# Kernel tuning notes

Hardware: AMD Instinct MI355X
Metric: run time of the kernel (lower is better)

Reference implementation:

```python
import jax, jax.numpy as jnp
import numpy as np

NU = 0.5

def _conv3x3(x, w):
    # x: [B,1,Hp,Wp] padded, w: [1,1,3,3]; VALID conv -> [B,1,H,W]
    return jax.lax.conv_general_dilated(
        x, w, window_strides=(1, 1), padding='VALID',
        dimension_numbers=('NCHW', 'OIHW', 'NCHW'))


def setup_inputs() -> dict:
    key = jax.random.key(0)
    k1, k2, k3, k4, k5 = jax.random.split(key, 5)
    B, H, W = 16, 1024, 1024
    u = jax.random.normal(k1, (B, 1, H, W), dtype=jnp.float32)
    u_vel = jax.random.normal(k2, (B, 1, H, W), dtype=jnp.float32)
    w1 = jax.random.normal(k3, (1, 1, 3, 3), dtype=jnp.float32)
    w2 = jax.random.normal(k4, (1, 1, 3, 3), dtype=jnp.float32)
    w3 = jax.random.normal(k5, (1, 1, 3, 3), dtype=jnp.float32)
    return {"u": u, "u_vel": u_vel, "w1": w1, "w2": w2, "w3": w3}


def reference(u, u_vel, w1, w2, w3):
    # replicate pad by 1 on H and W (torch 'replicate' == numpy 'edge')
    u_pad = jnp.pad(u, ((0, 0), (0, 0), (1, 1), (1, 1)), mode='edge')
    Lu = NU * _conv3x3(u_pad, w1) - u_vel * _conv3x3(u_pad, w2) - u_vel * _conv3x3(u_pad, w3)
    return Lu
```

## Files before the change

### kernel.cpp

```cpp
#include <hip/hip_runtime.h>


#define HH 1024
#define WW 1024
#define RPB 8
#define PPT 4
#define TPB (WW / PPT)

__global__ __launch_bounds__(TPB) void burgers_stencil(
    const float* __restrict__ u,
    const float* __restrict__ uvel,
    const float* __restrict__ w1,
    const float* __restrict__ w2,
    const float* __restrict__ w3,
    float* __restrict__ out,
    int rowBlocks)
{
    const int tid = threadIdx.x;
    const int b   = blockIdx.x / rowBlocks;
    const int y0  = (blockIdx.x % rowBlocks) * RPB;
    const int x0  = tid * PPT;

    float W1[9], W23[9];
#pragma unroll
    for (int i = 0; i < 9; ++i) {
        W1[i]  = w1[i];
        W23[i] = w2[i] + w3[i];
    }

    const size_t img = (size_t)b * HH * WW;
    const float* ub = u + img;

    float win[3][PPT + 2];

    auto loadrow = [&](int yr, float* dst) {
        yr = yr < 0 ? 0 : (yr > HH - 1 ? HH - 1 : yr);
        const float* row = ub + (size_t)yr * WW;
        const float4 v = *(const float4*)(row + x0);
        dst[1] = v.x; dst[2] = v.y; dst[3] = v.z; dst[4] = v.w;
        dst[0] = (x0 == 0)        ? v.x : row[x0 - 1];
        dst[5] = (x0 + PPT == WW) ? v.w : row[x0 + PPT];
    };

    loadrow(y0 - 1, win[0]);
    loadrow(y0,     win[1]);

    for (int r = 0; r < RPB; ++r) {
        const int y = y0 + r;
        loadrow(y + 1, win[2]);

        const float4 vv = *(const float4*)(uvel + img + (size_t)y * WW + x0);
        const float vel[PPT] = {vv.x, vv.y, vv.z, vv.w};

        float o[PPT];
#pragma unroll
        for (int j = 0; j < PPT; ++j) {
            float c1 = 0.f, c23 = 0.f;
#pragma unroll
            for (int rr = 0; rr < 3; ++rr) {
#pragma unroll
                for (int k = 0; k < 3; ++k) {
                    const float a = win[rr][j + k];
                    c1  = fmaf(W1[rr*3 + k],  a, c1);
                    c23 = fmaf(W23[rr*3 + k], a, c23);
                }
            }
            o[j] = 0.5f * c1 - vel[j] * c23;
        }
        float4 ov; ov.x = o[0]; ov.y = o[1]; ov.z = o[2]; ov.w = o[3];
        *(float4*)(out + img + (size_t)y * WW + x0) = ov;

#pragma unroll
        for (int k = 0; k < PPT + 2; ++k) {
            win[0][k] = win[1][k];
            win[1][k] = win[2][k];
        }
    }
}

extern "C" void kernel_launch(void* const* d_in, const int* in_sizes, int n_in,
                              void* d_out, int out_size, void* d_ws, size_t ws_size,
                              hipStream_t stream) {
    const float* u    = (const float*)d_in[0];
    const float* uvel = (const float*)d_in[1];
    const float* w1   = (const float*)d_in[2];
    const float* w2   = (const float*)d_in[3];
    const float* w3   = (const float*)d_in[4];
    float* out        = (float*)d_out;

    const int B = in_sizes[0] / (HH * WW);
    const int rowBlocks = HH / RPB;
    dim3 grid(B * rowBlocks);
    dim3 block(TPB);
    burgers_stencil<<<grid, block, 0, stream>>>(u, uvel, w1, w2, w3, out, rowBlocks);
}
```

Measured before the change: 180.8 us.

## Prefetch next rows, use wave shuffles for halos, make weights scalar

Software-pipelines the row loop so the u and u_vel loads for the next row are issued before the current row is computed, with the loop fully unrolled. The per-thread left and right halo loads are replaced by cross-lane shuffles, so only the edge lanes of each wavefront still load a halo element from global memory. Weights are forced into scalar registers with readfirstlane, and launch bounds request higher occupancy. This costs extra registers for the prefetch buffers and adds shuffle instructions, and the kernel is likely bandwidth-bound already.

```diff
diff --git a/kernel.cpp b/kernel.cpp
--- a/kernel.cpp
+++ b/kernel.cpp
@@ -7,7 +7,15 @@
 #define PPT 4
 #define TPB (WW / PPT)
 
-__global__ __launch_bounds__(TPB) void burgers_stencil(
+__device__ __forceinline__ float rfl(float x) {
+    union { float f; int i; } c; c.f = x;
+    c.i = __builtin_amdgcn_readfirstlane(c.i);
+    return c.f;
+}
+
+struct Row { float4 v; float el, er; };
+
+__global__ __launch_bounds__(TPB, 8) void burgers_stencil(
     const float* __restrict__ u,
     const float* __restrict__ uvel,
     const float* __restrict__ w1,
@@ -16,41 +24,64 @@
     float* __restrict__ out,
     int rowBlocks)
 {
-    const int tid = threadIdx.x;
-    const int b   = blockIdx.x / rowBlocks;
-    const int y0  = (blockIdx.x % rowBlocks) * RPB;
-    const int x0  = tid * PPT;
+    const int tid  = threadIdx.x;
+    const int lane = tid & 63;
+    const int b    = blockIdx.x / rowBlocks;
+    const int y0   = (blockIdx.x % rowBlocks) * RPB;
+    const int x0   = tid * PPT;
 
     float W1[9], W23[9];
 #pragma unroll
     for (int i = 0; i < 9; ++i) {
-        W1[i]  = w1[i];
-        W23[i] = w2[i] + w3[i];
+        W1[i]  = rfl(w1[i]);
+        W23[i] = rfl(w2[i] + w3[i]);
     }
 
     const size_t img = (size_t)b * HH * WW;
-    const float* ub = u + img;
+    const float* ub  = u + img;
+
+    auto issue_u = [&](int yr) -> Row {
+        yr = yr < 0 ? 0 : (yr > HH - 1 ? HH - 1 : yr);
+        const float* row = ub + (size_t)yr * WW;
+        Row r;
+        r.v  = *(const float4*)(row + x0);
+        r.el = 0.f; r.er = 0.f;
+        if (lane == 0  && x0 != 0)        r.el = row[x0 - 1];
+        if (lane == 63 && x0 + PPT != WW) r.er = row[x0 + PPT];
+        return r;
+    };
+
+    auto expand = [&](const Row& r, float* dst) {
+        const float4 v = r.v;
+        dst[1] = v.x; dst[2] = v.y; dst[3] = v.z; dst[4] = v.w;
+        float left  = __shfl_up(v.w, 1);
+        float right = __shfl_down(v.x, 1);
+        if (lane == 0)  left  = (x0 == 0)        ? v.x : r.el;
+        if (lane == 63) right = (x0 + PPT == WW) ? v.w : r.er;
+        dst[0] = left; dst[5] = right;
+    };
+
+    Row r0 = issue_u(y0 - 1);
+    Row r1 = issue_u(y0);
+    Row pu = issue_u(y0 + 1);
+    float4 pv = *(const float4*)(uvel + img + (size_t)y0 * WW + x0);
 
     float win[3][PPT + 2];
+    expand(r0, win[0]);
+    expand(r1, win[1]);
 
-    auto loadrow = [&](int yr, float* dst) {
-        yr = yr < 0 ? 0 : (yr > HH - 1 ? HH - 1 : yr);
-        const float* row = ub + (size_t)yr * WW;
-        const float4 v = *(const float4*)(row + x0);
-        dst[1] = v.x; dst[2] = v.y; dst[3] = v.z; dst[4] = v.w;
-        dst[0] = (x0 == 0)        ? v.x : row[x0 - 1];
-        dst[5] = (x0 + PPT == WW) ? v.w : row[x0 + PPT];
-    };
-
-    loadrow(y0 - 1, win[0]);
-    loadrow(y0,     win[1]);
-
+#pragma unroll
     for (int r = 0; r < RPB; ++r) {
         const int y = y0 + r;
-        loadrow(y + 1, win[2]);
 
-        const float4 vv = *(const float4*)(uvel + img + (size_t)y * WW + x0);
-        const float vel[PPT] = {vv.x, vv.y, vv.z, vv.w};
+        Row nu; float4 nv;
+        if (r < RPB - 1) {
+            nu = issue_u(y + 2);
+            nv = *(const float4*)(uvel + img + (size_t)(y + 1) * WW + x0);
+        }
+
+        expand(pu, win[2]);
+        const float vel[PPT] = {pv.x, pv.y, pv.z, pv.w};
 
         float o[PPT];
 #pragma unroll
@@ -75,6 +106,7 @@
             win[0][k] = win[1][k];
             win[1][k] = win[2][k];
         }
+        if (r < RPB - 1) { pu = nu; pv = nv; }
     }
 }
 
```

Result: no change. 179.5 us (-0.7%).

## Issue all stencil row loads upfront and uniformize weights via readfirstlane

Applied to the files above, without the earlier changes.

Rows per block drop from 8 to 4, and every input row (with halos) and every velocity row for the block is loaded at the start, before any compute. A schedule barrier keeps those loads grouped so their memory latency overlaps. The weights are made wave-uniform with readfirstlane so they can live in scalar registers. The cost is higher vector register pressure and more halo rows re-read per output row, since a block now covers 6 input rows for 4 outputs instead of 10 for 8.

```diff
diff --git a/kernel.cpp b/kernel.cpp
--- a/kernel.cpp
+++ b/kernel.cpp
@@ -3,9 +3,15 @@
 
 #define HH 1024
 #define WW 1024
-#define RPB 8
+#define RPB 4
 #define PPT 4
 #define TPB (WW / PPT)
+
+__device__ __forceinline__ float rfl(float x) {
+    union { float f; int i; } c; c.f = x;
+    c.i = __builtin_amdgcn_readfirstlane(c.i);
+    return c.f;
+}
 
 __global__ __launch_bounds__(TPB) void burgers_stencil(
     const float* __restrict__ u,
@@ -21,36 +27,48 @@
     const int y0  = (blockIdx.x % rowBlocks) * RPB;
     const int x0  = tid * PPT;
 
+    const size_t img = (size_t)b * HH * WW;
+    const float* ub  = u + img;
+
+    const int xl = (x0 == 0) ? 0 : x0 - 1;
+    const int xr = (x0 + PPT >= WW) ? WW - 1 : x0 + PPT;
+
+    float4 uv[RPB + 2]; float ul[RPB + 2], ur[RPB + 2];
+#pragma unroll
+    for (int i = 0; i < RPB + 2; ++i) {
+        int yr = y0 - 1 + i;
+        yr = yr < 0 ? 0 : (yr > HH - 1 ? HH - 1 : yr);
+        const float* row = ub + (size_t)yr * WW;
+        uv[i] = *(const float4*)(row + x0);
+        ul[i] = row[xl];
+        ur[i] = row[xr];
+    }
+    float4 vv[RPB];
+#pragma unroll
+    for (int r = 0; r < RPB; ++r)
+        vv[r] = *(const float4*)(uvel + img + (size_t)(y0 + r) * WW + x0);
+
     float W1[9], W23[9];
 #pragma unroll
     for (int i = 0; i < 9; ++i) {
-        W1[i]  = w1[i];
-        W23[i] = w2[i] + w3[i];
+        W1[i]  = rfl(w1[i]);
+        W23[i] = rfl(w2[i] + w3[i]);
     }
 
-    const size_t img = (size_t)b * HH * WW;
-    const float* ub = u + img;
+    __builtin_amdgcn_sched_barrier(0);
 
-    float win[3][PPT + 2];
-
-    auto loadrow = [&](int yr, float* dst) {
-        yr = yr < 0 ? 0 : (yr > HH - 1 ? HH - 1 : yr);
-        const float* row = ub + (size_t)yr * WW;
-        const float4 v = *(const float4*)(row + x0);
-        dst[1] = v.x; dst[2] = v.y; dst[3] = v.z; dst[4] = v.w;
-        dst[0] = (x0 == 0)        ? v.x : row[x0 - 1];
-        dst[5] = (x0 + PPT == WW) ? v.w : row[x0 + PPT];
-    };
-
-    loadrow(y0 - 1, win[0]);
-    loadrow(y0,     win[1]);
-
+#pragma unroll
     for (int r = 0; r < RPB; ++r) {
-        const int y = y0 + r;
-        loadrow(y + 1, win[2]);
-
-        const float4 vv = *(const float4*)(uvel + img + (size_t)y * WW + x0);
-        const float vel[PPT] = {vv.x, vv.y, vv.z, vv.w};
+        float p[3][PPT + 2];
+#pragma unroll
+        for (int rr = 0; rr < 3; ++rr) {
+            const int i = r + rr;
+            p[rr][0] = ul[i];
+            p[rr][1] = uv[i].x; p[rr][2] = uv[i].y;
+            p[rr][3] = uv[i].z; p[rr][4] = uv[i].w;
+            p[rr][5] = ur[i];
+        }
+        const float vel[PPT] = {vv[r].x, vv[r].y, vv[r].z, vv[r].w};
 
         float o[PPT];
 #pragma unroll
@@ -60,7 +78,7 @@
             for (int rr = 0; rr < 3; ++rr) {
 #pragma unroll
                 for (int k = 0; k < 3; ++k) {
-                    const float a = win[rr][j + k];
+                    const float a = p[rr][j + k];
                     c1  = fmaf(W1[rr*3 + k],  a, c1);
                     c23 = fmaf(W23[rr*3 + k], a, c23);
                 }
@@ -68,13 +86,7 @@
             o[j] = 0.5f * c1 - vel[j] * c23;
         }
         float4 ov; ov.x = o[0]; ov.y = o[1]; ov.z = o[2]; ov.w = o[3];
-        *(float4*)(out + img + (size_t)y * WW + x0) = ov;
-
-#pragma unroll
-        for (int k = 0; k < PPT + 2; ++k) {
-            win[0][k] = win[1][k];
-            win[1][k] = win[2][k];
-        }
+        *(float4*)(out + img + (size_t)(y0 + r) * WW + x0) = ov;
     }
 }
 
```

New measurement: 179.0 us. No clear change (-1.0%).
